# Kernel optimization log

Hardware: AMD Instinct MI355X
Metric: run time of the kernel (lower is better)

Reference implementation:

```python
import jax, jax.numpy as jnp
import numpy as np


def _grid_edges(H, W, diag):
    # Freudenthal triangulation edges: horizontal, vertical, and one diagonal per cell.
    idx = np.arange(H * W, dtype=np.int64).reshape(H, W)
    us = [idx[:, :-1].ravel(), idx[:-1, :].ravel()]
    vs = [idx[:, 1:].ravel(), idx[1:, :].ravel()]
    if diag == "main":
        us.append(idx[:-1, :-1].ravel()); vs.append(idx[1:, 1:].ravel())
    else:  # anti-diagonal = dual connectivity of the main-diagonal triangulation
        us.append(idx[1:, :-1].ravel()); vs.append(idx[:-1, 1:].ravel())
    return np.concatenate(us), np.concatenate(vs)


def _find(parent, x):
    r = x
    while parent[r] != r:
        r = parent[r]
    while parent[x] != r:  # path compression
        parent[x], x = r, parent[x]
    return r


def _sublevel_h0_pairs(g, u, v, boundary_idx=None):
    # 0-dim persistence of the sublevel (lower-star) filtration of vertex values g
    # over edge list (u, v); returns (birth_vertex, death_vertex) index pairs for all
    # FINITE bars (elder rule).  If boundary_idx is given, a virtual node at -inf is
    # attached to those vertices (models the unbounded outside region; never dies).
    n = g.shape[0]
    if boundary_idx is not None:
        u = np.concatenate([u, boundary_idx])
        v = np.concatenate([v, np.full(boundary_idx.shape[0], n, dtype=np.int64)])
        g = np.concatenate([g, np.array([-np.inf])])
    wu, wv = g[u], g[v]
    widx = np.where(wu >= wv, u, v)  # vertex whose value is the edge entry time
    order = np.argsort(np.maximum(wu, wv), kind="stable")
    parent = np.arange(g.shape[0], dtype=np.int64)
    birth = np.arange(g.shape[0], dtype=np.int64)  # component-min vertex per root
    pb, pd = [], []
    for ei in order:
        ra, rb = _find(parent, u[ei]), _find(parent, v[ei])
        if ra == rb:
            continue
        if g[birth[ra]] <= g[birth[rb]]:
            old, young = ra, rb
        else:
            old, young = rb, ra
        pb.append(birth[young]); pd.append(widx[ei])  # younger component dies here
        parent[young] = old
    return np.asarray(pb, dtype=np.int64), np.asarray(pd, dtype=np.int64)


def _toploss_pairs(f2d):
    # Critical-vertex pairs whose value differences make up the TopLoss value.
    H, W = f2d.shape
    f = f2d.ravel().astype(np.float64)
    # --- dim-0 superlevel persistence: sublevel union-find on -f ---
    u0, v0 = _grid_edges(H, W, "main")
    b0, d0 = _sublevel_h0_pairs(-f, u0, v0)  # b0: component argmax of f, d0: merge vertex
    # --- dim-1 superlevel persistence via Alexander duality:  H1({f>=t}) bars ---
    # correspond to H0 bars of the sublevel filtration of f on the dual connectivity,
    # with a virtual outside component attached to the image boundary.
    u1, v1 = _grid_edges(H, W, "anti")
    idx = np.arange(H * W, dtype=np.int64).reshape(H, W)
    boundary = np.unique(np.concatenate([idx[0], idx[-1], idx[:, 0], idx[:, -1]]))
    m_idx, M_idx = _sublevel_h0_pairs(f, u1, v1, boundary)
    # H1 bar = (birth f[M], death f[m]); PartialSumBarcodeLengths(dim=1, skip=1)
    # drops the single longest bar.
    L = f[M_idx] - f[m_idx]
    keep = np.argsort(-L, kind="stable")[1:]
    return b0, d0, M_idx[keep], m_idx[keep]


def setup_inputs() -> dict:
    key = jax.random.key(0)
    beta = jax.random.uniform(key, (256, 256), dtype=jnp.float32)
    return {"beta": beta}


def reference(beta):
    # pairing indices are a (piecewise-constant) function of the data; computed on host
    b0, d0, b1, d1 = _toploss_pairs(np.asarray(beta))
    fb = beta.ravel()
    # SumBarcodeLengths(dim=0): sum of finite H0 bar lengths (birth - death, superlevel)
    # + PartialSumBarcodeLengths(dim=1, skip=1): sum of all-but-longest H1 bar lengths
    return (fb[b0].sum() - fb[d0].sum()) + (fb[b1].sum() - fb[d1].sum())
```

## Files before the change

### kernel.cpp

```cpp
#include <hip/hip_runtime.h>

typedef unsigned int u32;
typedef unsigned short u16;
typedef unsigned long long u64;

#define NV 65536
#define TS 32
#define TVERTS 1024
#define TILES 64
#define SMAX 8192
#define VIRTID 8191
#define EMAX 65536


__global__ __launch_bounds__(1024) void k_tile(const float* __restrict__ f,
    u32* compD, u64* meD, float* maxD, double* partialT, u32* hdr, double* sumsG) {
  const int inst = blockIdx.z;
  const int bx = blockIdx.x;
  const int R0 = (bx >> 3) * TS, C0 = (bx & 7) * TS;
  const int tid = threadIdx.x;
  const int l = tid;
  const int lr = l >> 5, lc = l & 31;
  const int gr = R0 + lr, gc = C0 + lc;
  const int gv = gr * 256 + gc;

  __shared__ float sf[TVERTS];
  __shared__ u16 parL[TVERTS];
  __shared__ u64 meL[TVERTS];
  __shared__ u32 s_rank;
  __shared__ double s_red[16];
  __shared__ float s_redf[16];

  if (inst == 0 && bx == 0 && tid == 0) {
    hdr[0] = 0u; hdr[1] = 0u; hdr[2] = 0u; sumsG[0] = 0.0; sumsG[1] = 0.0;
  }
  if (tid < 128) meD[(size_t)inst * SMAX + (size_t)bx * 128 + tid] = ~0ull;
  if (tid == 0) s_rank = 0u;

  float x = f[gv];
  sf[l] = x; parL[l] = (u16)l;
  float fm = x;
  for (int o = 32; o > 0; o >>= 1) fm = fmaxf(fm, __shfl_down(fm, o));
  if ((tid & 63) == 0) s_redf[tid >> 6] = fm;
  __syncthreads();
  if (inst == 0 && tid == 0) {
    float m = s_redf[0];
    #pragma unroll
    for (int i = 1; i < 16; ++i) m = fmaxf(m, s_redf[i]);
    maxD[bx] = m;
  }

  auto amin = [](u64* slot, u64 p) {
    if (p < *slot) atomicMin(slot, p);
  };

  double wsum = 0.0;
  for (int round = 0; round < 14; ++round) {
    if (round > 0) {
      u32 xx = parL[l];
      for (int g = 0; g < TVERTS; ++g) { u32 p = parL[xx]; if (p == xx) break; xx = p; }
      parL[l] = (u16)xx;
      __syncthreads();
    }
    meL[l] = ~0ull;
    __syncthreads();
    {
      float fv = sf[l];
      u32 rv = parL[l];
      auto mk = [&](float w, int code) -> u64 {
        u32 kb = __float_as_uint(w); if (!inst) kb = ~kb;
        return ((u64)kb << 13) | (u64)(u32)(l << 3) | (u64)code;
      };
      auto pushI = [&](int nl, int code) {
        u32 rn = parL[nl];
        if (rn == rv) return;
        float w = inst ? fmaxf(fv, sf[nl]) : fminf(fv, sf[nl]);
        u64 p = mk(w, code);
        amin(&meL[rv], p); amin(&meL[rn], p);
      };
      auto pushO = [&](float fu, int code) {
        float w = inst ? fmaxf(fv, fu) : fminf(fv, fu);
        amin(&meL[rv], mk(w, code));
      };
      if (gc < 255) { if (lc < TS - 1) pushI(l + 1, 0); else pushO(f[gv + 1], 0); }
      if (gc > 0 && lc == 0) pushO(f[gv - 1], 4);
      if (gr < 255) { if (lr < TS - 1) pushI(l + TS, 1); else pushO(f[gv + 256], 1); }
      if (gr > 0 && lr == 0) pushO(f[gv - 256], 5);
      if (inst == 0) {
        if (gr < 255 && gc < 255) { if (lr < TS - 1 && lc < TS - 1) pushI(l + TS + 1, 2); else pushO(f[gv + 257], 2); }
        if (gr > 0 && gc > 0 && (lr == 0 || lc == 0)) pushO(f[gv - 257], 6);
      } else {
        if (gr > 0 && gc < 255) { if (lr > 0 && lc < TS - 1) pushI(l - TS + 1, 2); else pushO(f[gv - 255], 2); }
        if (gr < 255 && gc > 0 && (lr == TS - 1 || lc == 0)) pushO(f[gv + 255], 6);
        if (gr == 0 || gr == 255 || gc == 0 || gc == 255) {
          u32 kb = __float_as_uint(sf[l]);
          amin(&meL[rv], ((u64)kb << 13) | (u64)(u32)(l << 3) | 3ull);
        }
      }
    }
    __syncthreads();
    u32 dec = ~0u;
    bool did = false;
    if (parL[l] == (u16)l) {
      u64 m = meL[l];
      if (m != ~0ull) {
        int code = (int)(m & 7);
        if (code < 3) {
          int vL = (int)((m >> 3) & 0x3FF);
          int vlr = vL >> 5, vlc = vL & 31;
          int nl = -1;
          if (code == 0) { if (vlc < TS - 1) nl = vL + 1; }
          else if (code == 1) { if (vlr < TS - 1) nl = vL + TS; }
          else {
            if (inst == 0) { if (vlr < TS - 1 && vlc < TS - 1) nl = vL + TS + 1; }
            else           { if (vlr > 0 && vlc < TS - 1)      nl = vL - TS + 1; }
          }
          if (nl >= 0) {
            u32 r1 = parL[vL], r2 = parL[nl];
            u32 n = (r1 == (u32)l) ? r2 : r1;
            u64 mn = meL[n];
            if (!(mn == m && (u32)l < n)) {
              dec = n;
              u32 kb = (u32)(m >> 13); if (!inst) kb = ~kb;
              wsum += (double)__uint_as_float(kb);
              did = true;
            }
          }
        }
      }
    }
    int cnt = __syncthreads_count(did ? 1 : 0);
    if (dec != ~0u) parL[l] = (u16)dec;
    __syncthreads();
    if (cnt == 0) break;
  }
  if (parL[l] == (u16)l) meL[l] = (u64)atomicAdd(&s_rank, 1u);
  __syncthreads();
  {
    u32 xx = parL[l];
    for (int g = 0; g < TVERTS; ++g) { u32 p = parL[xx]; if (p == xx) break; xx = p; }
    compD[(size_t)inst * NV + gv] = (u32)(bx * 128) + (u32)meL[xx];
  }
  double wt = wsum;
  for (int o = 32; o > 0; o >>= 1) wt += __shfl_down(wt, o);
  if ((tid & 63) == 0) s_red[tid >> 6] = wt;
  __syncthreads();
  if (tid == 0) {
    double t = 0.0;
    #pragma unroll
    for (int i = 0; i < 16; ++i) t += s_red[i];
    partialT[inst * 64 + bx] = t;
  }
}

__global__ __launch_bounds__(256) void k_emit(const float* __restrict__ f,
    const u32* __restrict__ compD, u32* hdr, u64* eb, u64* meD) {
  const int inst = blockIdx.z;
  const u32* __restrict__ cd = compD + (size_t)inst * NV;
  u64* eo = eb + (size_t)inst * 2 * EMAX;
  u64* me = meD + (size_t)inst * SMAX;
  const int tid = threadIdx.x;
  const int lane = tid & 63;
  int v = blockIdx.x * 256 + tid;
  int gr = v >> 8, gc = v & 255;
  float fv = f[v];
  u32 c0 = cd[v];

  __shared__ u64 s_ed[1024];
  __shared__ u32 s_cnt, s_base;
  if (tid == 0) s_cnt = 0u;
  __syncthreads();

  auto emit = [&](bool has, u32 key, u32 c1) {
    u64 pack = 0;
    if (has) {
      pack = ((u64)key << 26) | ((u64)c0 << 13) | (u64)c1;
      if (pack < me[c0]) atomicMin(&me[c0], pack);
      if (pack < me[c1]) atomicMin(&me[c1], pack);
    }
    u64 mask = __ballot(has);
    if (mask == 0) return;
    int lead = __ffsll((long long)mask) - 1;
    u32 base = 0;
    if (lane == lead) base = atomicAdd(&s_cnt, (u32)__popcll(mask));
    base = __shfl(base, lead);
    if (has) s_ed[base + (u32)__popcll(mask & ((1ull << lane) - 1ull))] = pack;
  };
  { bool has = false; u32 key = 0, c1 = 0;
    if (gc < 255) { c1 = cd[v + 1]; if (c1 != c0) { float w = inst ? fmaxf(fv, f[v + 1]) : fminf(fv, f[v + 1]); key = __float_as_uint(w); if (!inst) key = ~key; has = true; } }
    emit(has, key, c1); }
  { bool has = false; u32 key = 0, c1 = 0;
    if (gr < 255) { c1 = cd[v + 256]; if (c1 != c0) { float w = inst ? fmaxf(fv, f[v + 256]) : fminf(fv, f[v + 256]); key = __float_as_uint(w); if (!inst) key = ~key; has = true; } }
    emit(has, key, c1); }
  { bool has = false; u32 key = 0, c1 = 0;
    if (inst == 0) { if (gr < 255 && gc < 255) { c1 = cd[v + 257]; if (c1 != c0) { key = ~__float_as_uint(fminf(fv, f[v + 257])); has = true; } } }
    else { if (gr > 0 && gc < 255) { c1 = cd[v - 255]; if (c1 != c0) { key = __float_as_uint(fmaxf(fv, f[v - 255])); has = true; } } }
    emit(has, key, c1); }
  { bool has = false; u32 key = 0;
    if (inst == 1 && (gr == 0 || gr == 255 || gc == 0 || gc == 255)) { key = __float_as_uint(fv); has = true; }
    emit(has, key, (u32)VIRTID); }

  __syncthreads();
  if (tid == 0) s_base = s_cnt ? atomicAdd(&hdr[inst], s_cnt) : 0u;
  __syncthreads();
  u32 n = s_cnt, base = s_base;
  for (u32 i = tid; i < n; i += 256) {
    u32 idx = base + i;
    if (idx < EMAX) eo[idx] = s_ed[i];
  }
}

__global__ __launch_bounds__(1024) void k_bor(const u32* __restrict__ hdr_ro,
    u64* eb, const u64* __restrict__ meD, const double* __restrict__ partialT,
    const float* __restrict__ maxD, double* sumsG, u32* done, float* out) {
  const int inst = blockIdx.z;
  const int tid = threadIdx.x;
  const int lane = tid & 63;
  u32 E = hdr_ro[inst]; if (E > EMAX) E = EMAX;
  u64* cur = eb + (size_t)inst * 2 * EMAX;
  u64* nxt = cur + EMAX;

  __shared__ u16 parL[SMAX];
  __shared__ u64 meL[SMAX];
  __shared__ u16 actL[SMAX];
  __shared__ u32 s_cnt, s_act;
  __shared__ double s_red[16];
  __shared__ float s_mv;

  if (tid == 0) s_act = 0u;
  for (u32 s = tid; s < SMAX; s += 1024) parL[s] = (u16)s;
  __syncthreads();
  for (u32 s = tid; s < SMAX; s += 1024) {
    u64 m = meD[(size_t)inst * SMAX + s];
    meL[s] = m;
    if (m != ~0ull) { u32 a = atomicAdd(&s_act, 1u); actL[a] = (u16)s; }
  }
  __syncthreads();
  u32 A = s_act;
  double wsum = 0.0;

  for (int round = 0; round < 32 && A > 0 && E > 0; ++round) {
    for (u32 a = tid; a < A; a += 1024) {
      u32 s = actL[a]; u64 m = meL[s];
      u32 lo = (u32)(m >> 13) & 0x1FFFu, hi = (u32)m & 0x1FFFu;
      u32 n = (lo == s) ? hi : lo;
      u64 mn = meL[n];
      if (mn == m && s < n) continue;
      parL[s] = (u16)n;
      u32 kb = (u32)(m >> 26); if (!inst) kb = ~kb;
      wsum += (double)__uint_as_float(kb);
    }
    if (tid == 0) { s_cnt = 0u; s_act = 0u; }
    __syncthreads();
    for (u32 a = tid; a < A; a += 1024) {
      u32 s = actL[a];
      u32 x = parL[s];
      for (int g = 0; g < SMAX; ++g) { u32 p = parL[x]; if (p == x) break; x = p; }
      parL[s] = (u16)x;
      meL[s] = ~0ull;
    }
    __syncthreads();
    u32 Epad = (E + 1023u) & ~1023u;
    for (u32 e = tid; e < Epad; e += 1024) {
      bool alive = false; u64 np = 0; u32 rl = 0, rh = 0;
      if (e < E) {
        u64 w = cur[e];
        u32 lo = (u32)(w >> 13) & 0x1FFFu, hi = (u32)w & 0x1FFFu;
        rl = parL[lo]; rh = parL[hi];
        if (rl != rh) { alive = true; np = (w & ~(u64)0x3FFFFFFull) | ((u64)rl << 13) | (u64)rh; }
      }
      u64 mask = __ballot(alive);
      if (mask) {
        int lead = __ffsll((long long)mask) - 1;
        u32 base = 0;
        if (lane == lead) base = atomicAdd(&s_cnt, (u32)__popcll(mask));
        base = __shfl(base, lead);
        if (alive) {
          u32 ni = base + (u32)__popcll(mask & ((1ull << lane) - 1ull));
          nxt[ni] = np;
          if (np < meL[rl]) { u64 old = atomicMin(&meL[rl], np);
            if (old == ~0ull) { u32 a = atomicAdd(&s_act, 1u); actL[a] = (u16)rl; } }
          if (np < meL[rh]) { u64 old = atomicMin(&meL[rh], np);
            if (old == ~0ull) { u32 a = atomicAdd(&s_act, 1u); actL[a] = (u16)rh; } }
        }
      }
    }
    __syncthreads();
    E = s_cnt; A = s_act;
    u64* t = cur; cur = nxt; nxt = t;
  }

  double wt = wsum;
  for (int o = 32; o > 0; o >>= 1) wt += __shfl_down(wt, o);
  if (lane == 0) s_red[tid >> 6] = wt;
  __syncthreads();
  if (tid < 64) {
    float m = maxD[tid];
    for (int o = 32; o > 0; o >>= 1) m = fmaxf(m, __shfl_down(m, o));
    if (tid == 0) s_mv = m;
  }
  double v = 0.0;
  if (tid < 64) {
    v = partialT[inst * 64 + tid];
    if (tid < 16) v += s_red[tid];
    for (int o = 32; o > 0; o >>= 1) v += __shfl_down(v, o);
  }
  __syncthreads();
  if (tid == 0) {
    double total = v;
    atomicExch((u64*)&sumsG[inst], (u64)__double_as_longlong(total));
    __threadfence();
    u32 d = atomicAdd(done, 1u);
    if (d == 1u) {
      __threadfence();
      u64 ob = atomicAdd((u64*)&sumsG[1 - inst], 0ull);
      double other = __longlong_as_double((long long)ob);
      double w0 = (inst == 0) ? total : other;
      double w1 = (inst == 1) ? total : other;
      out[0] = (float)(w1 - w0 - (double)s_mv);
    }
  }
}

extern "C" void kernel_launch(void* const* d_in, const int* in_sizes, int n_in,
                              void* d_out, int out_size, void* d_ws, size_t ws_size,
                              hipStream_t stream) {
  const float* f = (const float*)d_in[0];
  float* out = (float*)d_out;
  char* ws = (char*)d_ws;
  double* sumsG    = (double*)ws;
  u32* hdr         = (u32*)(ws + 16);
  float* maxD      = (float*)(ws + 64);
  double* partialT = (double*)(ws + 512);
  u32* compD       = (u32*)(ws + 2048);
  u64* eb          = (u64*)(ws + 526336);
  u64* meD         = (u64*)(ws + 2623488);

  k_tile<<<dim3(TILES, 1, 2), dim3(1024), 0, stream>>>(f, compD, meD, maxD,
                                                       partialT, hdr, sumsG);
  k_emit<<<dim3(256, 1, 2), dim3(256), 0, stream>>>(f, compD, hdr, eb, meD);
  k_bor<<<dim3(1, 1, 2), dim3(1024), 0, stream>>>(hdr, eb, meD, partialT, maxD,
                                                  sumsG, hdr + 2, out);
}
```

Baseline: 106.8 us.

## Tag per-round min-edges and finish Boruvka tail in a single wavefront

The Boruvka merge loop drops its separate pointer-jumping pass and its meL reset barrier. Each round's min-edge candidates now carry a descending 6-bit tag in the top bits, so stale entries are recognised without clearing, and roots are found lazily with path compression during edge relabeling. Once the live edge count drops to 1024 or fewer, the remaining rounds run in one 64-lane wavefront with no __syncthreads, avoiding block-wide barriers on small tail rounds. The risks are that the tag limits the round count and that lazy root finding can walk longer chains.

```diff
diff --git a/kernel.cpp b/kernel.cpp
--- a/kernel.cpp
+++ b/kernel.cpp
@@ -11,6 +11,7 @@
 #define SMAX 8192
 #define VIRTID 8191
 #define EMAX 65536
+#define TAILE 1024
 
 
 __global__ __launch_bounds__(1024) void k_tile(const float* __restrict__ f,
@@ -174,7 +175,7 @@
   auto emit = [&](bool has, u32 key, u32 c1) {
     u64 pack = 0;
     if (has) {
-      pack = ((u64)key << 26) | ((u64)c0 << 13) | (u64)c1;
+      pack = (62ull << 58) | ((u64)key << 26) | ((u64)c0 << 13) | (u64)c1;
       if (pack < me[c0]) atomicMin(&me[c0], pack);
       if (pack < me[c1]) atomicMin(&me[c1], pack);
     }
@@ -225,7 +226,6 @@
   __shared__ u16 actL[SMAX];
   __shared__ u32 s_cnt, s_act;
   __shared__ double s_red[16];
-  __shared__ float s_mv;
 
   if (tid == 0) s_act = 0u;
   for (u32 s = tid; s < SMAX; s += 1024) parL[s] = (u16)s;
@@ -233,41 +233,42 @@
   for (u32 s = tid; s < SMAX; s += 1024) {
     u64 m = meD[(size_t)inst * SMAX + s];
     meL[s] = m;
-    if (m != ~0ull) { u32 a = atomicAdd(&s_act, 1u); actL[a] = (u16)s; }
+    if ((m >> 58) == 62ull) { u32 a = atomicAdd(&s_act, 1u); actL[a] = (u16)s; }
   }
   __syncthreads();
   u32 A = s_act;
+  u64 curtag = 62;
   double wsum = 0.0;
 
-  for (int round = 0; round < 32 && A > 0 && E > 0; ++round) {
+  auto rootOf = [&](u32 x) -> u32 {
+    u32 x0 = x;
+    for (int g = 0; g < SMAX; ++g) { u32 p = parL[x]; if (p == x) break; x = p; }
+    if (parL[x0] != (u16)x) parL[x0] = (u16)x;
+    return x;
+  };
+
+  for (int round = 0; round < 40 && A > 0 && E > TAILE; ++round) {
     for (u32 a = tid; a < A; a += 1024) {
       u32 s = actL[a]; u64 m = meL[s];
       u32 lo = (u32)(m >> 13) & 0x1FFFu, hi = (u32)m & 0x1FFFu;
       u32 n = (lo == s) ? hi : lo;
-      u64 mn = meL[n];
-      if (mn == m && s < n) continue;
+      if (meL[n] == m && s < n) continue;
       parL[s] = (u16)n;
       u32 kb = (u32)(m >> 26); if (!inst) kb = ~kb;
       wsum += (double)__uint_as_float(kb);
     }
     if (tid == 0) { s_cnt = 0u; s_act = 0u; }
     __syncthreads();
-    for (u32 a = tid; a < A; a += 1024) {
-      u32 s = actL[a];
-      u32 x = parL[s];
-      for (int g = 0; g < SMAX; ++g) { u32 p = parL[x]; if (p == x) break; x = p; }
-      parL[s] = (u16)x;
-      meL[s] = ~0ull;
-    }
-    __syncthreads();
+    u64 newtag = curtag - 1;
     u32 Epad = (E + 1023u) & ~1023u;
     for (u32 e = tid; e < Epad; e += 1024) {
       bool alive = false; u64 np = 0; u32 rl = 0, rh = 0;
       if (e < E) {
         u64 w = cur[e];
-        u32 lo = (u32)(w >> 13) & 0x1FFFu, hi = (u32)w & 0x1FFFu;
-        rl = parL[lo]; rh = parL[hi];
-        if (rl != rh) { alive = true; np = (w & ~(u64)0x3FFFFFFull) | ((u64)rl << 13) | (u64)rh; }
+        rl = rootOf((u32)(w >> 13) & 0x1FFFu);
+        rh = rootOf((u32)w & 0x1FFFu);
+        if (rl != rh)
+          { alive = true; np = (newtag << 58) | ((u64)(u32)(w >> 26) << 26) | ((u64)rl << 13) | (u64)rh; }
       }
       u64 mask = __ballot(alive);
       if (mask) {
@@ -279,35 +280,77 @@
           u32 ni = base + (u32)__popcll(mask & ((1ull << lane) - 1ull));
           nxt[ni] = np;
           if (np < meL[rl]) { u64 old = atomicMin(&meL[rl], np);
-            if (old == ~0ull) { u32 a = atomicAdd(&s_act, 1u); actL[a] = (u16)rl; } }
+            if ((old >> 58) != newtag) { u32 a = atomicAdd(&s_act, 1u); actL[a] = (u16)rl; } }
           if (np < meL[rh]) { u64 old = atomicMin(&meL[rh], np);
-            if (old == ~0ull) { u32 a = atomicAdd(&s_act, 1u); actL[a] = (u16)rh; } }
+            if ((old >> 58) != newtag) { u32 a = atomicAdd(&s_act, 1u); actL[a] = (u16)rh; } }
         }
       }
     }
     __syncthreads();
-    E = s_cnt; A = s_act;
+    E = s_cnt; A = s_act; curtag = newtag;
     u64* t = cur; cur = nxt; nxt = t;
   }
 
-  double wt = wsum;
-  for (int o = 32; o > 0; o >>= 1) wt += __shfl_down(wt, o);
-  if (lane == 0) s_red[tid >> 6] = wt;
-  __syncthreads();
-  if (tid < 64) {
-    float m = maxD[tid];
-    for (int o = 32; o > 0; o >>= 1) m = fmaxf(m, __shfl_down(m, o));
-    if (tid == 0) s_mv = m;
-  }
-  double v = 0.0;
-  if (tid < 64) {
-    v = partialT[inst * 64 + tid];
-    if (tid < 16) v += s_red[tid];
-    for (int o = 32; o > 0; o >>= 1) v += __shfl_down(v, o);
-  }
-  __syncthreads();
-  if (tid == 0) {
-    double total = v;
+  {
+    double wt = wsum;
+    for (int o = 32; o > 0; o >>= 1) wt += __shfl_down(wt, o);
+    if (lane == 0) s_red[tid >> 6] = wt;
+  }
+  __syncthreads();
+  if (tid >= 64) return;
+  wsum = 0.0;
+
+  for (int round = 0; round < 40 && A > 0; ++round) {
+    for (u32 a = lane; a < A; a += 64) {
+      u32 s = actL[a]; u64 m = meL[s];
+      u32 lo = (u32)(m >> 13) & 0x1FFFu, hi = (u32)m & 0x1FFFu;
+      u32 n = (lo == s) ? hi : lo;
+      if (meL[n] == m && s < n) continue;
+      parL[s] = (u16)n;
+      u32 kb = (u32)(m >> 26); if (!inst) kb = ~kb;
+      wsum += (double)__uint_as_float(kb);
+    }
+    if (lane == 0) { s_cnt = 0u; s_act = 0u; }
+    u64 newtag = curtag - 1;
+    u32 Epad = (E + 63u) & ~63u;
+    for (u32 e = lane; e < Epad; e += 64) {
+      bool alive = false; u64 np = 0; u32 rl = 0, rh = 0;
+      if (e < E) {
+        u64 w = cur[e];
+        rl = rootOf((u32)(w >> 13) & 0x1FFFu);
+        rh = rootOf((u32)w & 0x1FFFu);
+        if (rl != rh)
+          { alive = true; np = (newtag << 58) | ((u64)(u32)(w >> 26) << 26) | ((u64)rl << 13) | (u64)rh; }
+      }
+      u64 mask = __ballot(alive);
+      if (mask) {
+        int lead = __ffsll((long long)mask) - 1;
+        u32 base = 0;
+        if (lane == lead) base = atomicAdd(&s_cnt, (u32)__popcll(mask));
+        base = __shfl(base, lead);
+        if (alive) {
+          u32 ni = base + (u32)__popcll(mask & ((1ull << lane) - 1ull));
+          nxt[ni] = np;
+          if (np < meL[rl]) { u64 old = atomicMin(&meL[rl], np);
+            if ((old >> 58) != newtag) { u32 a = atomicAdd(&s_act, 1u); actL[a] = (u16)rl; } }
+          if (np < meL[rh]) { u64 old = atomicMin(&meL[rh], np);
+            if ((old >> 58) != newtag) { u32 a = atomicAdd(&s_act, 1u); actL[a] = (u16)rh; } }
+        }
+      }
+    }
+    E = s_cnt; A = s_act; curtag = newtag;
+    u64* t = cur; cur = nxt; nxt = t;
+  }
+
+  double wt2 = wsum;
+  for (int o = 32; o > 0; o >>= 1) wt2 += __shfl_down(wt2, o);
+  float m = maxD[lane];
+  for (int o = 32; o > 0; o >>= 1) m = fmaxf(m, __shfl_down(m, o));
+  double v = partialT[inst * 64 + lane];
+  if (lane < 16) v += s_red[lane];
+  for (int o = 32; o > 0; o >>= 1) v += __shfl_down(v, o);
+  if (lane == 0) {
+    double total = v + wt2;
     atomicExch((u64*)&sumsG[inst], (u64)__double_as_longlong(total));
     __threadfence();
     u32 d = atomicAdd(done, 1u);
@@ -317,7 +360,7 @@
       double other = __longlong_as_double((long long)ob);
       double w0 = (inst == 0) ? total : other;
       double w1 = (inst == 1) ? total : other;
-      out[0] = (float)(w1 - w0 - (double)s_mv);
+      out[0] = (float)(w1 - w0 - (double)m);
     }
   }
 }
```

Measured after the change: 143.5 us. 34.4% more time.

## Replace active-list tracking in Boruvka loop with round-tagged min-edge keys

Applied to the files above, without the earlier changes.

The Boruvka merge kernel no longer keeps a shared active-component list built with atomics. Instead each packed min-edge value carries a round tag in its top bits, and every pass scans all supernode slots, skipping non-roots and entries whose tag is stale. This removes the per-round resets of meL and the atomicAdd list appends, and it also merges the final reduction blocks to drop a barrier. In exchange, every round scans the full SMAX range rather than only active entries, and the round cap is raised from 32 to 40.

```diff
diff --git a/kernel.cpp b/kernel.cpp
--- a/kernel.cpp
+++ b/kernel.cpp
@@ -174,7 +174,7 @@
   auto emit = [&](bool has, u32 key, u32 c1) {
     u64 pack = 0;
     if (has) {
-      pack = ((u64)key << 26) | ((u64)c0 << 13) | (u64)c1;
+      pack = (62ull << 58) | ((u64)key << 26) | ((u64)c0 << 13) | (u64)c1;
       if (pack < me[c0]) atomicMin(&me[c0], pack);
       if (pack < me[c1]) atomicMin(&me[c1], pack);
     }
@@ -222,52 +222,48 @@
 
   __shared__ u16 parL[SMAX];
   __shared__ u64 meL[SMAX];
-  __shared__ u16 actL[SMAX];
-  __shared__ u32 s_cnt, s_act;
+  __shared__ u32 s_cnt;
   __shared__ double s_red[16];
-  __shared__ float s_mv;
-
-  if (tid == 0) s_act = 0u;
-  for (u32 s = tid; s < SMAX; s += 1024) parL[s] = (u16)s;
-  __syncthreads();
+
   for (u32 s = tid; s < SMAX; s += 1024) {
-    u64 m = meD[(size_t)inst * SMAX + s];
-    meL[s] = m;
-    if (m != ~0ull) { u32 a = atomicAdd(&s_act, 1u); actL[a] = (u16)s; }
-  }
-  __syncthreads();
-  u32 A = s_act;
+    parL[s] = (u16)s;
+    meL[s] = meD[(size_t)inst * SMAX + s];
+  }
+  __syncthreads();
+  u64 curtag = 62;
   double wsum = 0.0;
 
-  for (int round = 0; round < 32 && A > 0 && E > 0; ++round) {
-    for (u32 a = tid; a < A; a += 1024) {
-      u32 s = actL[a]; u64 m = meL[s];
+  for (int round = 0; round < 40 && E > 0; ++round) {
+    for (u32 s = tid; s < SMAX; s += 1024) {
+      if (parL[s] != (u16)s) continue;
+      u64 m = meL[s];
+      if ((m >> 58) != curtag) continue;
       u32 lo = (u32)(m >> 13) & 0x1FFFu, hi = (u32)m & 0x1FFFu;
       u32 n = (lo == s) ? hi : lo;
-      u64 mn = meL[n];
-      if (mn == m && s < n) continue;
+      if (meL[n] == m && s < n) continue;
       parL[s] = (u16)n;
       u32 kb = (u32)(m >> 26); if (!inst) kb = ~kb;
       wsum += (double)__uint_as_float(kb);
     }
-    if (tid == 0) { s_cnt = 0u; s_act = 0u; }
-    __syncthreads();
-    for (u32 a = tid; a < A; a += 1024) {
-      u32 s = actL[a];
+    if (tid == 0) s_cnt = 0u;
+    __syncthreads();
+    for (u32 s = tid; s < SMAX; s += 1024) {
       u32 x = parL[s];
+      if (parL[x] == (u16)x) continue;
       for (int g = 0; g < SMAX; ++g) { u32 p = parL[x]; if (p == x) break; x = p; }
       parL[s] = (u16)x;
-      meL[s] = ~0ull;
-    }
-    __syncthreads();
+    }
+    __syncthreads();
+    u64 newtag = curtag - 1;
     u32 Epad = (E + 1023u) & ~1023u;
     for (u32 e = tid; e < Epad; e += 1024) {
       bool alive = false; u64 np = 0; u32 rl = 0, rh = 0;
       if (e < E) {
         u64 w = cur[e];
-        u32 lo = (u32)(w >> 13) & 0x1FFFu, hi = (u32)w & 0x1FFFu;
-        rl = parL[lo]; rh = parL[hi];
-        if (rl != rh) { alive = true; np = (w & ~(u64)0x3FFFFFFull) | ((u64)rl << 13) | (u64)rh; }
+        rl = parL[(u32)(w >> 13) & 0x1FFFu];
+        rh = parL[(u32)w & 0x1FFFu];
+        if (rl != rh)
+          { alive = true; np = (newtag << 58) | ((u64)(u32)(w >> 26) << 26) | ((u64)rl << 13) | (u64)rh; }
       }
       u64 mask = __ballot(alive);
       if (mask) {
@@ -278,15 +274,13 @@
         if (alive) {
           u32 ni = base + (u32)__popcll(mask & ((1ull << lane) - 1ull));
           nxt[ni] = np;
-          if (np < meL[rl]) { u64 old = atomicMin(&meL[rl], np);
-            if (old == ~0ull) { u32 a = atomicAdd(&s_act, 1u); actL[a] = (u16)rl; } }
-          if (np < meL[rh]) { u64 old = atomicMin(&meL[rh], np);
-            if (old == ~0ull) { u32 a = atomicAdd(&s_act, 1u); actL[a] = (u16)rh; } }
+          if (np < meL[rl]) atomicMin(&meL[rl], np);
+          if (np < meL[rh]) atomicMin(&meL[rh], np);
         }
       }
     }
     __syncthreads();
-    E = s_cnt; A = s_act;
+    E = s_cnt; curtag = newtag;
     u64* t = cur; cur = nxt; nxt = t;
   }
 
@@ -297,27 +291,22 @@
   if (tid < 64) {
     float m = maxD[tid];
     for (int o = 32; o > 0; o >>= 1) m = fmaxf(m, __shfl_down(m, o));
-    if (tid == 0) s_mv = m;
-  }
-  double v = 0.0;
-  if (tid < 64) {
-    v = partialT[inst * 64 + tid];
+    double v = partialT[inst * 64 + tid];
     if (tid < 16) v += s_red[tid];
     for (int o = 32; o > 0; o >>= 1) v += __shfl_down(v, o);
-  }
-  __syncthreads();
-  if (tid == 0) {
-    double total = v;
-    atomicExch((u64*)&sumsG[inst], (u64)__double_as_longlong(total));
-    __threadfence();
-    u32 d = atomicAdd(done, 1u);
-    if (d == 1u) {
+    if (tid == 0) {
+      double total = v;
+      atomicExch((u64*)&sumsG[inst], (u64)__double_as_longlong(total));
       __threadfence();
-      u64 ob = atomicAdd((u64*)&sumsG[1 - inst], 0ull);
-      double other = __longlong_as_double((long long)ob);
-      double w0 = (inst == 0) ? total : other;
-      double w1 = (inst == 1) ? total : other;
-      out[0] = (float)(w1 - w0 - (double)s_mv);
+      u32 d = atomicAdd(done, 1u);
+      if (d == 1u) {
+        __threadfence();
+        u64 ob = atomicAdd((u64*)&sumsG[1 - inst], 0ull);
+        double other = __longlong_as_double((long long)ob);
+        double w0 = (inst == 0) ? total : other;
+        double w1 = (inst == 1) ? total : other;
+        out[0] = (float)(w1 - w0 - (double)m);
+      }
     }
   }
 }
```

Result: slower. 119.3 us (+11.7%).
